# Optimization experiments

Hardware: AMD Instinct MI355X
Metric: run time of the kernel (lower is better)

## Reference

```python
import jax, jax.numpy as jnp
import numpy as np

INPUT_DIM = 1068   # 768 + 300
HIDDEN = 768
KERNEL_SIZES = (3, 5, 7)
NUM_KERNELS = (256, 256, 256)
SPACE = 16
NEG_SLOPE = 0.01   # LeakyReLU default
N_DOCS = 128
MAX_LEN = 200


def _pos_encoding(n_pos, d):
    pos = np.arange(n_pos)[:, None].astype(np.float32)
    i = np.arange(d // 2)[None, :].astype(np.float32)
    angle = pos / np.power(10000.0, 2.0 * i / d)
    pe = np.zeros((n_pos, d), dtype=np.float32)
    pe[:, 0::2] = np.sin(angle)
    pe[:, 1::2] = np.cos(angle)
    return pe

_PE = jnp.asarray(_pos_encoding(MAX_LEN, INPUT_DIM))


def _lstm_cell(x, h, c, W_ih, W_hh, b_ih, b_hh):
    # torch.nn.LSTMCell gate math, gate order i, f, g, o
    g = x @ W_ih.T + b_ih + h @ W_hh.T + b_hh
    i, f, gg, o = jnp.split(g, 4, axis=-1)
    c2 = jax.nn.sigmoid(f) * c + jax.nn.sigmoid(i) * jnp.tanh(gg)
    return jax.nn.sigmoid(o) * jnp.tanh(c2), c2


def _chunked_hidden(xp, W_ih, W_hh, b_ih, b_hh):
    # Replicates getHiddenStates: each chunk of SPACE positions is one batched
    # LSTMCell step; the state at offset j within a chunk carries to offset j of
    # the next chunk (SPACE interleaved recurrences). Padding the tail is safe
    # because padded states are never read back (original slices hx[:len]).
    N, F = xp.shape
    H = W_hh.shape[1]
    n_chunks = -(-N // SPACE)
    pad = n_chunks * SPACE - N
    xk = jnp.pad(xp, ((0, pad), (0, 0))).reshape(n_chunks, SPACE, F)

    def step(carry, xc):
        h, c = carry
        h, c = _lstm_cell(xc, h, c, W_ih, W_hh, b_ih, b_hh)
        return (h, c), (h, c)

    init = (jnp.zeros((SPACE, H), xp.dtype), jnp.zeros((SPACE, H), xp.dtype))
    _, (hs, cs) = jax.lax.scan(step, init, xk)
    return hs.reshape(-1, H)[:N], cs.reshape(-1, H)[:N]


def _maxpool_same(x, k):  # x: [C, L], stride 1, padding k//2 (k odd -> same L)
    p = k // 2
    return jax.lax.reduce_window(x, -jnp.inf, jax.lax.max, (1, k), (1, 1), [(0, 0), (p, p)])


def setup_inputs() -> dict:
    key = jax.random.key(0)
    ks = jax.random.split(key, 16)
    doc_lens = np.asarray(jax.random.randint(ks[0], (N_DOCS,), 50, MAX_LEN))
    L = N_DOCS * MAX_LEN
    inp = {
        "x": jax.random.normal(ks[1], (1, L, INPUT_DIM), jnp.float32),
        "doc_lens": doc_lens,
    }
    for j, (k, oc) in enumerate(zip(KERNEL_SIZES, NUM_KERNELS)):
        inp[f"conv_w{j}"] = jax.random.normal(ks[2 + j], (oc, INPUT_DIM, k), jnp.float32) * 0.02
        inp[f"conv_b{j}"] = jnp.zeros((oc,), jnp.float32)
    F = sum(NUM_KERNELS)
    for name, kk in (("", ks[6]), ("_rev", ks[7])):
        k1, k2 = jax.random.split(kk)
        inp[f"W_ih{name}"] = jax.random.normal(k1, (4 * HIDDEN, F), jnp.float32) * 0.05
        inp[f"W_hh{name}"] = jax.random.normal(k2, (4 * HIDDEN, HIDDEN), jnp.float32) * 0.05
        inp[f"b_ih{name}"] = jnp.zeros((4 * HIDDEN,), jnp.float32)
        inp[f"b_hh{name}"] = jnp.zeros((4 * HIDDEN,), jnp.float32)
    return inp


def reference(x, doc_lens, conv_w0, conv_b0, conv_w1, conv_b1, conv_w2, conv_b2,
              W_ih, W_hh, b_ih, b_hh, W_ih_rev, W_hh_rev, b_ih_rev, b_hh_rev):
    doc_lens = np.asarray(doc_lens)
    N = int(doc_lens.sum())
    pos_idx = np.concatenate([np.arange(int(l)) for l in doc_lens])  # per-doc positions

    x_doc = x[0, :N] + _PE[pos_idx]                 # [N, D]
    xc = x_doc.T[None]                              # [1, D, N]

    convs, pools = [], []
    for w, b, k in ((conv_w0, conv_b0, 3), (conv_w1, conv_b1, 5), (conv_w2, conv_b2, 7)):
        p = (k - 1) // 2  # 'same' padding for odd k
        y = jax.lax.conv_general_dilated(xc, w, (1,), [(p, p)],
                                         dimension_numbers=("NCH", "OIH", "NCH"))[0] + b[:, None]
        y = jnp.where(y >= 0, y, NEG_SLOPE * y)     # LeakyReLU
        convs.append(y)
        pools.append(_maxpool_same(y, k))
    x_feat = jnp.concatenate(convs, axis=0).T       # [N, sumK]
    x_pooled = jnp.concatenate(pools, axis=0).T     # [N, sumK]

    h, c = _chunked_hidden(x_pooled, W_ih, W_hh, b_ih, b_hh)
    # NOTE: the original also runs getHiddenStates on the reversed sequence with
    # lstm_rev (h_rev, c_rev) but never uses the result -> dead code, omitted.

    min_dis = SPACE // 2 + 1
    z = jnp.zeros((min_dis, HIDDEN), h.dtype)
    h_prev = jnp.concatenate([z, h[:N - min_dis]], axis=0)   # h[i-min_dis] or 0
    c_prev = jnp.concatenate([z, c[:N - min_dis]], axis=0)
    h_next = jnp.concatenate([h[min_dis:], z], axis=0)       # h[i+min_dis] or 0
    c_next = jnp.concatenate([c[min_dis:], z], axis=0)

    hi, _ = _lstm_cell(x_feat, h_prev, c_prev, W_ih, W_hh, b_ih, b_hh)
    hi_rev, _ = _lstm_cell(x_feat, h_next, c_next, W_ih_rev, W_hh_rev, b_ih_rev, b_hh_rev)
    return jnp.concatenate([hi, hi_rev], axis=-1)[None]      # [1, N, 2H]
```

## Files before the change

kernel.cpp:

```cpp
#include <hip/hip_runtime.h>
#include <hip/hip_bf16.h>
#include <hip/hip_fp16.h>
#include <math.h>

#define DIN   1068
#define DPAD  1088
#define HID   768
#define G4    3072
#define NWG_SCAN 96
#define SLAB  2048
#define HPAD  776
#define GBM   128
#define GBN   128
#define AROWP 40

typedef _Float16 half8 __attribute__((ext_vector_type(8)));
typedef float    floatx4 __attribute__((ext_vector_type(4)));

__device__ __forceinline__ float sigf(float x){ return 1.0f/(1.0f + expf(-x)); }

__global__ void k_prep(const int* __restrict__ doc_lens, int* __restrict__ pos_idx, int N){
    __shared__ int off[129];
    if (threadIdx.x == 0){
        int a = 0;
        for (int d = 0; d < 128; ++d){ off[d] = a; a += doc_lens[d]; }
        off[128] = a;
    }
    __syncthreads();
    for (int d = threadIdx.x; d < 128; d += blockDim.x){
        int s = off[d], e = off[d+1];
        for (int n = s; n < e && n < N; ++n) pos_idx[n] = n - s;
    }
}

__global__ void k_fill_xdoc(const float* __restrict__ x, const int* __restrict__ pos_idx,
                            float* __restrict__ xd, int N){
    int idx = blockIdx.x*256 + threadIdx.x;
    int total = N * DPAD;
    if (idx >= total) return;
    int n = idx / DPAD;
    int d = idx - n*DPAD;
    float v = 0.f;
    if (d < DIN){
        int pos = pos_idx[n];
        int i2 = d & ~1;
        float ex  = expf(-(float)i2 * (9.210340371976184f / 1068.0f));
        float ang = (float)pos * ex;
        v = x[(size_t)n*DIN + d] + ((d & 1) ? cosf(ang) : sinf(ang));
    }
    xd[(size_t)(n+4)*DPAD + d] = v;
}

__global__ void k_repack_w(const float* __restrict__ w0, const float* __restrict__ w1,
                           const float* __restrict__ w2, float* __restrict__ wrep){
    int idx = blockIdx.x*256 + threadIdx.x;
    const int total = 15*256*DPAD;
    if (idx >= total) return;
    int d    = idx % DPAD;
    int rest = idx / DPAD;
    int oc   = rest % 256;
    int tau  = rest / 256;
    const float* w; int k, t;
    if (tau < 3)      { w = w0; k = 3; t = tau;     }
    else if (tau < 8) { w = w1; k = 5; t = tau - 3; }
    else              { w = w2; k = 7; t = tau - 8; }
    float v = 0.f;
    if (d < DIN) v = w[((size_t)oc*DIN + d)*k + t];
    wrep[(size_t)idx] = v;
}

template<bool SPLIT>
__device__ __forceinline__ void mfma_core(
    const float* __restrict__ A, const float* __restrict__ B, int K,
    int m0, int shift, int rowcap, int tid, floatx4 (&acc)[4][4],
    _Float16* __restrict__ Ahi, _Float16* __restrict__ Alo,
    _Float16* __restrict__ Bhi, _Float16* __restrict__ Blo)
{
    const int st_r = tid >> 1;
    const int st_s = (tid & 1) * 16;
    const int wv = tid >> 6, lane = tid & 63;
    const int wr = wv >> 1, wc = wv & 1;
    const int mloc = lane & 15, kb = lane >> 4;
    for (int k0 = 0; k0 < K; k0 += 32){
        {
            float av[16] = {};
            int r = m0 + st_r + shift;
            if ((unsigned)r < (unsigned)rowcap){
                const float* pa = A + (size_t)r*K + k0 + st_s;
                *(float4*)&av[0]  = *(const float4*)pa;
                *(float4*)&av[4]  = *(const float4*)(pa+4);
                *(float4*)&av[8]  = *(const float4*)(pa+8);
                *(float4*)&av[12] = *(const float4*)(pa+12);
            }
            #pragma unroll
            for (int g = 0; g < 2; ++g){
                half8 hh, hl;
                #pragma unroll
                for (int e = 0; e < 8; ++e){
                    float f = av[g*8+e];
                    _Float16 h = (_Float16)f;
                    hh[e] = h;
                    if (SPLIT) hl[e] = (_Float16)(f - (float)h);
                }
                *(half8*)&Ahi[st_r*AROWP + st_s + g*8] = hh;
                if (SPLIT) *(half8*)&Alo[st_r*AROWP + st_s + g*8] = hl;
            }
        }
        {
            float bv[16];
            const float* pb = B + (size_t)st_r*K + k0 + st_s;
            *(float4*)&bv[0]  = *(const float4*)pb;
            *(float4*)&bv[4]  = *(const float4*)(pb+4);
            *(float4*)&bv[8]  = *(const float4*)(pb+8);
            *(float4*)&bv[12] = *(const float4*)(pb+12);
            #pragma unroll
            for (int g = 0; g < 2; ++g){
                half8 hh, hl;
                #pragma unroll
                for (int e = 0; e < 8; ++e){
                    float f = bv[g*8+e];
                    _Float16 h = (_Float16)f;
                    hh[e] = h;
                    if (SPLIT) hl[e] = (_Float16)(f - (float)h);
                }
                *(half8*)&Bhi[st_r*AROWP + st_s + g*8] = hh;
                if (SPLIT) *(half8*)&Blo[st_r*AROWP + st_s + g*8] = hl;
            }
        }
        __syncthreads();
        half8 afh[4], bfh[4], afl[4], bfl[4];
        #pragma unroll
        for (int i = 0; i < 4; ++i){
            afh[i] = *(const half8*)&Ahi[(wr*64 + i*16 + mloc)*AROWP + kb*8];
            bfh[i] = *(const half8*)&Bhi[(wc*64 + i*16 + mloc)*AROWP + kb*8];
            if (SPLIT){
                afl[i] = *(const half8*)&Alo[(wr*64 + i*16 + mloc)*AROWP + kb*8];
                bfl[i] = *(const half8*)&Blo[(wc*64 + i*16 + mloc)*AROWP + kb*8];
            }
        }
        #pragma unroll
        for (int i = 0; i < 4; ++i)
            #pragma unroll
            for (int j = 0; j < 4; ++j){
                acc[i][j] = __builtin_amdgcn_mfma_f32_16x16x32_f16(afh[i], bfh[j], acc[i][j], 0, 0, 0);
                if (SPLIT){
                    acc[i][j] = __builtin_amdgcn_mfma_f32_16x16x32_f16(afh[i], bfl[j], acc[i][j], 0, 0, 0);
                    acc[i][j] = __builtin_amdgcn_mfma_f32_16x16x32_f16(afl[i], bfh[j], acc[i][j], 0, 0, 0);
                }
            }
        __syncthreads();
    }
}

template<bool CHALF>
__global__ __launch_bounds__(256) void k_gemm_split(
    const float* __restrict__ A0, const float* __restrict__ B0,
    const float* __restrict__ bias0, const float* __restrict__ bias1,
    void* __restrict__ C, int M, int K, int ldc)
{
    __shared__ _Float16 Ahi[GBM*AROWP], Alo[GBM*AROWP];
    __shared__ _Float16 Bhi[GBN*AROWP], Blo[GBN*AROWP];
    floatx4 zz = {0.f, 0.f, 0.f, 0.f};
    floatx4 acc[4][4];
    #pragma unroll
    for (int i = 0; i < 4; ++i)
        #pragma unroll
        for (int j = 0; j < 4; ++j) acc[i][j] = zz;
    const int tid = threadIdx.x;
    const int m0 = blockIdx.x*GBM;
    const int n0 = blockIdx.y*GBN;
    mfma_core<true>(A0, B0 + (size_t)n0*K, K, m0, 0, M, tid, acc, Ahi, Alo, Bhi, Blo);
    const int wv = tid >> 6, lane = tid & 63;
    const int wr = wv >> 1, wc = wv & 1;
    const int mloc = lane & 15, kb = lane >> 4;
    float bv[4];
    #pragma unroll
    for (int j = 0; j < 4; ++j){
        int cn = n0 + wc*64 + j*16 + mloc;
        bv[j] = bias0[cn] + (bias1 ? bias1[cn] : 0.f);
    }
    #pragma unroll
    for (int i = 0; i < 4; ++i){
        #pragma unroll
        for (int r = 0; r < 4; ++r){
            int gm = m0 + wr*64 + i*16 + kb*4 + r;
            if (gm >= M) continue;
            #pragma unroll
            for (int j = 0; j < 4; ++j){
                int cn = n0 + wc*64 + j*16 + mloc;
                float v = acc[i][j][r] + bv[j];
                if (CHALF) ((__half*)C)[(size_t)gm*ldc + cn] = __float2half(v);
                else       ((float*)C)[(size_t)gm*ldc + cn] = v;
            }
        }
    }
}

__global__ __launch_bounds__(256) void k_gemm_plain2(
    const float* __restrict__ A0, const float* __restrict__ B0,
    const float* __restrict__ A1, const float* __restrict__ B1,
    const float* __restrict__ bias0, const float* __restrict__ bias1,
    float* __restrict__ C, int M, int K, int ldc)
{
    __shared__ _Float16 Ahi[GBM*AROWP];
    __shared__ _Float16 Bhi[GBN*AROWP];
    floatx4 zz = {0.f, 0.f, 0.f, 0.f};
    floatx4 acc[4][4];
    #pragma unroll
    for (int i = 0; i < 4; ++i)
        #pragma unroll
        for (int j = 0; j < 4; ++j) acc[i][j] = zz;
    const int tid = threadIdx.x;
    const int m0 = blockIdx.x*GBM;
    const int n0 = blockIdx.y*GBN;
    mfma_core<false>(A0, B0 + (size_t)n0*K, K, m0, 0, M, tid, acc, Ahi, nullptr, Bhi, nullptr);
    mfma_core<false>(A1, B1 + (size_t)n0*K, K, m0, 0, M, tid, acc, Ahi, nullptr, Bhi, nullptr);
    const int wv = tid >> 6, lane = tid & 63;
    const int wr = wv >> 1, wc = wv & 1;
    const int mloc = lane & 15, kb = lane >> 4;
    float bv[4];
    #pragma unroll
    for (int j = 0; j < 4; ++j){
        int cn = n0 + wc*64 + j*16 + mloc;
        bv[j] = bias0[cn] + bias1[cn];
    }
    #pragma unroll
    for (int i = 0; i < 4; ++i){
        #pragma unroll
        for (int r = 0; r < 4; ++r){
            int gm = m0 + wr*64 + i*16 + kb*4 + r;
            if (gm >= M) continue;
            #pragma unroll
            for (int j = 0; j < 4; ++j){
                int cn = n0 + wc*64 + j*16 + mloc;
                C[(size_t)gm*ldc + cn] = acc[i][j][r] + bv[j];
            }
        }
    }
}

__global__ __launch_bounds__(256) void k_conv_gemm(
    const float* __restrict__ xd, const float* __restrict__ wrep,
    const float* __restrict__ cb0, const float* __restrict__ cb1, const float* __restrict__ cb2,
    float* __restrict__ x_feat, int N)
{
    __shared__ _Float16 Ahi[GBM*AROWP], Alo[GBM*AROWP];
    __shared__ _Float16 Bhi[GBN*AROWP], Blo[GBN*AROWP];
    floatx4 zz = {0.f, 0.f, 0.f, 0.f};
    floatx4 acc[4][4];
    #pragma unroll
    for (int i = 0; i < 4; ++i)
        #pragma unroll
        for (int j = 0; j < 4; ++j) acc[i][j] = zz;
    const int tid = threadIdx.x;
    const int m0  = blockIdx.x*GBM;
    const int gid = blockIdx.y;
    const int g = gid >> 1, half = gid & 1;
    const int kg = (g==0)?3:((g==1)?5:7);
    const int p  = kg >> 1;
    const int tb = (g==0)?0:((g==1)?3:8);
    for (int t = 0; t < kg; ++t){
        const float* B = wrep + ((size_t)(tb + t)*256 + half*128)*DPAD;
        mfma_core<true>(xd, B, DPAD, m0, 4 + t - p, N + 8, tid, acc, Ahi, Alo, Bhi, Blo);
    }
    const float* cb = (g==0)?cb0:((g==1)?cb1:cb2);
    const int wv = tid >> 6, lane = tid & 63;
    const int wr = wv >> 1, wc = wv & 1;
    const int mloc = lane & 15, kb = lane >> 4;
    float bv[4];
    #pragma unroll
    for (int j = 0; j < 4; ++j) bv[j] = cb[half*128 + wc*64 + j*16 + mloc];
    const int colbase = g*256 + half*128 + wc*64 + mloc;
    #pragma unroll
    for (int i = 0; i < 4; ++i){
        #pragma unroll
        for (int r = 0; r < 4; ++r){
            int gm = m0 + wr*64 + i*16 + kb*4 + r;
            if (gm >= N) continue;
            float* crow = x_feat + (size_t)gm*HID + colbase;
            #pragma unroll
            for (int j = 0; j < 4; ++j){
                float y = acc[i][j][r] + bv[j];
                crow[j*16] = (y >= 0.f) ? y : 0.01f*y;
            }
        }
    }
}

__global__ void k_pool(const float* __restrict__ xf, float* __restrict__ xp, int N){
    int idx = blockIdx.x*256 + threadIdx.x;
    if (idx >= N*HID) return;
    int n = idx / HID, ch = idx - n*HID;
    int p = (ch < 256) ? 1 : ((ch < 512) ? 2 : 3);
    float m = -INFINITY;
    for (int d = -p; d <= p; ++d){
        int r = n + d;
        if (0 <= r && r < N) m = fmaxf(m, xf[(size_t)r*HID + ch]);
    }
    xp[idx] = m;
}

__global__ __launch_bounds__(256, 1) void k_scan(
    const __half* __restrict__ G1, const float* __restrict__ W_hh,
    float* __restrict__ h_all, __half* __restrict__ c_all,
    __half* __restrict__ h_buf, unsigned int* __restrict__ flags,
    int N, int n_chunks)
{
    __shared__ __align__(16) __half hs16[16*HPAD];
    __shared__ float gbuf[2][32][17];
    const int w    = blockIdx.x;
    const int t    = threadIdx.x;
    const int lane = t & 63;
    const int wv   = t >> 6;
    const int mt   = wv & 1;
    const int kh   = wv >> 1;
    const int mloc = lane & 15;
    const int kb   = lane >> 4;
    const int mg   = mt*16 + mloc;
    const int qq   = mg >> 3;
    const int il   = mg & 7;
    const int grow = qq*HID + w*8 + il;
    half8 areg[12];
    #pragma unroll
    for (int sk = 0; sk < 12; ++sk){
        const float* wp = W_hh + (size_t)grow*HID + kh*384 + sk*32 + kb*8;
        half8 a;
        #pragma unroll
        for (int e = 0; e < 8; ++e) a[e] = (_Float16)wp[e];
        areg[sk] = a;
    }
    float cstate = 0.f;
    const int ci = t >> 4;
    const int cc = t & 15;
    const int st_row = t >> 4;
    const int st_wq  = (t & 15) * 12;
    for (int s = 0; s < n_chunks; ++s){
        float g1v0=0.f, g1v1=0.f, g1v2=0.f, g1v3=0.f;
        int n = s*16 + cc;
        if (t < 128 && n < N){
            const __half* g1r = G1 + (size_t)n*G4 + w*8 + ci;
            g1v0 = __half2float(g1r[0]);
            g1v1 = __half2float(g1r[HID]);
            g1v2 = __half2float(g1r[2*HID]);
            g1v3 = __half2float(g1r[3*HID]);
        }
        {
            const unsigned long long* hsrc =
                (const unsigned long long*)(h_buf + (size_t)(s & 1)*(16*HID))
                + (size_t)st_row*192 + st_wq;
            unsigned long long tmp[12];
            #pragma unroll
            for (int i = 0; i < 12; ++i)
                tmp[i] = __hip_atomic_load(hsrc + i, __ATOMIC_RELAXED,
                                           __HIP_MEMORY_SCOPE_AGENT);
            unsigned long long* hrow =
                (unsigned long long*)(hs16 + (size_t)st_row*HPAD) + st_wq;
            #pragma unroll
            for (int i = 0; i < 12; ++i) hrow[i] = tmp[i];
        }
        __syncthreads();
        {
            floatx4 acc = {0.f, 0.f, 0.f, 0.f};
            const _Float16* hb = (const _Float16*)hs16;
            #pragma unroll
            for (int sk = 0; sk < 12; ++sk){
                int k0 = kh*384 + sk*32 + kb*8;
                half8 b = *(const half8*)(hb + (size_t)mloc*HPAD + k0);
                acc = __builtin_amdgcn_mfma_f32_16x16x32_f16(areg[sk], b, acc, 0, 0, 0);
            }
            #pragma unroll
            for (int r = 0; r < 4; ++r)
                gbuf[kh][mt*16 + kb*4 + r][mloc] = acc[r];
        }
        __syncthreads();
        if (t < 128 && n < N){
            int col = w*8 + ci;
            float gI = gbuf[0][0*8+ci][cc] + gbuf[1][0*8+ci][cc] + g1v0;
            float gF = gbuf[0][1*8+ci][cc] + gbuf[1][1*8+ci][cc] + g1v1;
            float gG = gbuf[0][2*8+ci][cc] + gbuf[1][2*8+ci][cc] + g1v2;
            float gO = gbuf[0][3*8+ci][cc] + gbuf[1][3*8+ci][cc] + g1v3;
            float c2 = sigf(gF)*cstate + sigf(gI)*tanhf(gG);
            float h2 = sigf(gO)*tanhf(c2);
            cstate = c2;
            size_t rowoff = (size_t)(16 + n)*HID + col;
            h_all[rowoff] = h2;
            c_all[rowoff] = __float2half(c2);
            unsigned hb2 = (unsigned)__half_as_ushort(__float2half(h2));
            unsigned other = __shfl_xor(hb2, 16, 64);
            if ((ci & 1) == 0){
                unsigned pk = hb2 | (other << 16);
                unsigned* dst = (unsigned*)h_buf +
                    (((size_t)((s+1)&1)*(16*HID) + (size_t)cc*HID + col) >> 1);
                __hip_atomic_store(dst, pk, __ATOMIC_RELAXED, __HIP_MEMORY_SCOPE_AGENT);
            }
        }
        __syncthreads();
        if (t == 0)
            __hip_atomic_store(&flags[w*16], (unsigned)(s + 1),
                               __ATOMIC_RELAXED, __HIP_MEMORY_SCOPE_AGENT);
        if (t < NWG_SCAN){
            while (__hip_atomic_load(&flags[t*16], __ATOMIC_RELAXED,
                                     __HIP_MEMORY_SCOPE_AGENT) < (unsigned)(s + 1))
                __builtin_amdgcn_s_sleep(1);
        }
        __syncthreads();
    }
}

__global__ void k_cell(const float* __restrict__ g2, const float* __restrict__ g3,
                       const __half* __restrict__ c_all, float* __restrict__ out,
                       int n0, int Mslab, int N){
    int idx = blockIdx.x*256 + threadIdx.x;
    if (idx >= Mslab*HID) return;
    int nl = idx / HID, j = idx - nl*HID;
    int n = n0 + nl;
    const float* r2 = g2 + (size_t)nl*G4;
    float cp = __half2float(c_all[(size_t)(7 + n)*HID + j]);
    float c2 = sigf(r2[HID + j])*cp + sigf(r2[j])*tanhf(r2[2*HID + j]);
    out[(size_t)n*1536 + j] = sigf(r2[3*HID + j])*tanhf(c2);
    const float* r3 = g3 + (size_t)nl*G4;
    float cn = __half2float(c_all[(size_t)(25 + n)*HID + j]);
    float c3 = sigf(r3[HID + j])*cn + sigf(r3[j])*tanhf(r3[2*HID + j]);
    out[(size_t)n*1536 + HID + j] = sigf(r3[3*HID + j])*tanhf(c3);
}

extern "C" void kernel_launch(void* const* d_in, const int* in_sizes, int n_in,
                              void* d_out, int out_size, void* d_ws, size_t ws_size,
                              hipStream_t stream)
{
    const float* x     = (const float*)d_in[0];
    const int*   dl    = (const int*)  d_in[1];
    const float* cw0   = (const float*)d_in[2];
    const float* cb0   = (const float*)d_in[3];
    const float* cw1   = (const float*)d_in[4];
    const float* cb1   = (const float*)d_in[5];
    const float* cw2   = (const float*)d_in[6];
    const float* cb2   = (const float*)d_in[7];
    const float* W_ih  = (const float*)d_in[8];
    const float* W_hh  = (const float*)d_in[9];
    const float* b_ih  = (const float*)d_in[10];
    const float* b_hh  = (const float*)d_in[11];
    const float* W_ihr = (const float*)d_in[12];
    const float* W_hhr = (const float*)d_in[13];
    const float* b_ihr = (const float*)d_in[14];
    const float* b_hhr = (const float*)d_in[15];
    float* out = (float*)d_out;
    (void)in_sizes; (void)n_in;
    const int N = out_size / (2*HID);
    if (N <= 0) return;
    const int n_chunks = (N + 15)/16;
    const int N16 = n_chunks*16;

    auto AL = [](size_t b){ return (b + 255) & ~(size_t)255; };
    const size_t szXd   = AL((size_t)(N+8)*DPAD*4);
    const size_t szW    = AL((size_t)15*256*DPAD*4);
    const size_t szPool = AL((size_t)N*HID*4);
    const size_t szH    = AL((size_t)(N+32)*HID*4);
    const size_t szC    = AL((size_t)(N+32)*HID*2);
    size_t r0 = szXd + szW;
    if (szPool     > r0) r0 = szPool;
    if (szH + szC  > r0) r0 = szH + szC;
    const size_t szF    = AL((size_t)N*HID*4);
    size_t szG1 = AL((size_t)N16*G4*2);
    const size_t szGG   = AL((size_t)SLAB*G4*4);
    if (2*szGG > szG1) szG1 = 2*szGG;
    const size_t szHB   = AL((size_t)2*16*HID*2);
    const size_t szFL   = AL((size_t)NWG_SCAN*16*4);
    const size_t szPI   = AL((size_t)N*4);

    char* wsb = (char*)d_ws;
    size_t off = 0;
    char* R0   = wsb;              off += r0;
    char* pF   = wsb + off;        off += szF;
    char* pG1  = wsb + off;        off += szG1;
    char* pHB  = wsb + off;        off += szHB;
    char* pFL  = wsb + off;        off += szFL;
    char* pPI  = wsb + off;        off += szPI;
    if (off > ws_size) return;

    float*          xd    = (float*)R0;
    float*          wrep  = (float*)(R0 + szXd);
    float*          x_pool= (float*)R0;
    float*          h_all = (float*)R0;
    __half*         c_all = (__half*)(R0 + szH);
    float*          x_feat= (float*)pF;
    __half*         G1    = (__half*)pG1;
    float*          g2    = (float*)pG1;
    float*          g3    = (float*)(pG1 + szGG);
    __half*         h_buf = (__half*)pHB;
    unsigned*       flags = (unsigned*)pFL;
    int*            pos_idx = (int*)pPI;

    hipMemsetAsync(xd, 0, (size_t)4*DPAD*4, stream);
    hipMemsetAsync(xd + (size_t)(N+4)*DPAD, 0, (size_t)4*DPAD*4, stream);
    k_prep<<<1, 128, 0, stream>>>(dl, pos_idx, N);
    k_fill_xdoc<<<(N*DPAD + 255)/256, 256, 0, stream>>>(x, pos_idx, xd, N);
    k_repack_w<<<(15*256*DPAD + 255)/256, 256, 0, stream>>>(cw0, cw1, cw2, wrep);

    const int mt = (N + GBM - 1)/GBM;
    k_conv_gemm<<<dim3(mt, 6), 256, 0, stream>>>(xd, wrep, cb0, cb1, cb2, x_feat, N);
    k_pool<<<(N*HID + 255)/256, 256, 0, stream>>>(x_feat, x_pool, N);

    k_gemm_split<true><<<dim3(mt, G4/GBN), 256, 0, stream>>>(
        x_pool, W_ih, b_ih, b_hh, G1, N, HID, G4);

    hipMemsetAsync(h_all, 0, (size_t)16*HID*4, stream);
    hipMemsetAsync(h_all + (size_t)(16+N)*HID, 0, (size_t)16*HID*4, stream);
    hipMemsetAsync(c_all, 0, (size_t)16*HID*2, stream);
    hipMemsetAsync(c_all + (size_t)(16+N)*HID, 0, (size_t)16*HID*2, stream);
    hipMemsetAsync(h_buf, 0, (size_t)2*16*HID*2, stream);
    hipMemsetAsync(flags, 0, szFL, stream);
    k_scan<<<NWG_SCAN, 256, 0, stream>>>(G1, W_hh, h_all, c_all, h_buf, flags, N, n_chunks);

    for (int n0 = 0; n0 < N; n0 += SLAB){
        int ms  = (N - n0 < SLAB) ? (N - n0) : SLAB;
        int mts = (ms + GBM - 1)/GBM;
        k_gemm_plain2<<<dim3(mts, G4/GBN), 256, 0, stream>>>(
            x_feat + (size_t)n0*HID, W_ih, h_all + (size_t)(7+n0)*HID, W_hh,
            b_ih, b_hh, g2, ms, HID, G4);
        k_gemm_plain2<<<dim3(mts, G4/GBN), 256, 0, stream>>>(
            x_feat + (size_t)n0*HID, W_ihr, h_all + (size_t)(25+n0)*HID, W_hhr,
            b_ihr, b_hhr, g3, ms, HID, G4);
        k_cell<<<(ms*HID + 255)/256, 256, 0, stream>>>(g2, g3, c_all, out, n0, ms, N);
    }
}
```

Baseline: 6.606 ms.

## Replace per-step flag barrier with step-tagged hidden-state words in scan

The recurrent scan kernel no longer synchronises its 96 workgroups with a flag array, a spin loop and two extra block barriers per step. Each packed fp16 hidden pair is now stored together with its step number in one 64-bit atomic word, and readers spin until every word they need carries the expected tag. This removes a global barrier round trip from the serial critical path. In exchange the hidden-state buffer doubles in size and each thread polls 24 words instead of one flag.

Measured after the change: 15.87 ms. +140.2%, slower.

```diff
diff --git a/kernel.cpp b/kernel.cpp
--- a/kernel.cpp
+++ b/kernel.cpp
@@ -303,7 +303,7 @@
 __global__ __launch_bounds__(256, 1) void k_scan(
     const __half* __restrict__ G1, const float* __restrict__ W_hh,
     float* __restrict__ h_all, __half* __restrict__ c_all,
-    __half* __restrict__ h_buf, unsigned int* __restrict__ flags,
+    unsigned long long* __restrict__ h_buf,
     int N, int n_chunks)
 {
     __shared__ __align__(16) __half hs16[16*HPAD];
@@ -333,7 +333,6 @@
     const int ci = t >> 4;
     const int cc = t & 15;
     const int st_row = t >> 4;
-    const int st_wq  = (t & 15) * 12;
     for (int s = 0; s < n_chunks; ++s){
         float g1v0=0.f, g1v1=0.f, g1v2=0.f, g1v3=0.f;
         int n = s*16 + cc;
@@ -345,18 +344,32 @@
             g1v3 = __half2float(g1r[3*HID]);
         }
         {
-            const unsigned long long* hsrc =
-                (const unsigned long long*)(h_buf + (size_t)(s & 1)*(16*HID))
-                + (size_t)st_row*192 + st_wq;
-            unsigned long long tmp[12];
+            const unsigned want = (unsigned)s;
+            const unsigned long long* src =
+                h_buf + (size_t)(s & 1)*6144 + (size_t)t*24;
+            unsigned long long v[24];
+            #pragma unroll
+            for (int i = 0; i < 24; ++i)
+                v[i] = __hip_atomic_load(src + i, __ATOMIC_RELAXED,
+                                         __HIP_MEMORY_SCOPE_AGENT);
+            for (;;){
+                bool ok = true;
+                #pragma unroll
+                for (int i = 0; i < 24; ++i)
+                    ok &= ((unsigned)(v[i] >> 32) == want);
+                if (ok) break;
+                __builtin_amdgcn_s_sleep(1);
+                #pragma unroll
+                for (int i = 0; i < 24; ++i)
+                    if ((unsigned)(v[i] >> 32) != want)
+                        v[i] = __hip_atomic_load(src + i, __ATOMIC_RELAXED,
+                                                 __HIP_MEMORY_SCOPE_AGENT);
+            }
+            unsigned long long* hrow =
+                (unsigned long long*)(hs16 + (size_t)st_row*HPAD) + (t & 15)*12;
             #pragma unroll
             for (int i = 0; i < 12; ++i)
-                tmp[i] = __hip_atomic_load(hsrc + i, __ATOMIC_RELAXED,
-                                           __HIP_MEMORY_SCOPE_AGENT);
-            unsigned long long* hrow =
-                (unsigned long long*)(hs16 + (size_t)st_row*HPAD) + st_wq;
-            #pragma unroll
-            for (int i = 0; i < 12; ++i) hrow[i] = tmp[i];
+                hrow[i] = (v[2*i] & 0xffffffffull) | (v[2*i+1] << 32);
         }
         __syncthreads();
         {
@@ -373,37 +386,35 @@
                 gbuf[kh][mt*16 + kb*4 + r][mloc] = acc[r];
         }
         __syncthreads();
-        if (t < 128 && n < N){
-            int col = w*8 + ci;
-            float gI = gbuf[0][0*8+ci][cc] + gbuf[1][0*8+ci][cc] + g1v0;
-            float gF = gbuf[0][1*8+ci][cc] + gbuf[1][1*8+ci][cc] + g1v1;
-            float gG = gbuf[0][2*8+ci][cc] + gbuf[1][2*8+ci][cc] + g1v2;
-            float gO = gbuf[0][3*8+ci][cc] + gbuf[1][3*8+ci][cc] + g1v3;
-            float c2 = sigf(gF)*cstate + sigf(gI)*tanhf(gG);
-            float h2 = sigf(gO)*tanhf(c2);
-            cstate = c2;
-            size_t rowoff = (size_t)(16 + n)*HID + col;
-            h_all[rowoff] = h2;
-            c_all[rowoff] = __float2half(c2);
+        if (t < 128){
+            float h2 = 0.f;
+            if (n < N){
+                int col = w*8 + ci;
+                float gI = gbuf[0][0*8+ci][cc] + gbuf[1][0*8+ci][cc] + g1v0;
+                float gF = gbuf[0][1*8+ci][cc] + gbuf[1][1*8+ci][cc] + g1v1;
+                float gG = gbuf[0][2*8+ci][cc] + gbuf[1][2*8+ci][cc] + g1v2;
+                float gO = gbuf[0][3*8+ci][cc] + gbuf[1][3*8+ci][cc] + g1v3;
+                float c2 = sigf(gF)*cstate + sigf(gI)*tanhf(gG);
+                h2 = sigf(gO)*tanhf(c2);
+                cstate = c2;
+                size_t rowoff = (size_t)(16 + n)*HID + col;
+                h_all[rowoff] = h2;
+                c_all[rowoff] = __float2half(c2);
+            }
             unsigned hb2 = (unsigned)__half_as_ushort(__float2half(h2));
             unsigned other = __shfl_xor(hb2, 16, 64);
             if ((ci & 1) == 0){
                 unsigned pk = hb2 | (other << 16);
-                unsigned* dst = (unsigned*)h_buf +
-                    (((size_t)((s+1)&1)*(16*HID) + (size_t)cc*HID + col) >> 1);
-                __hip_atomic_store(dst, pk, __ATOMIC_RELAXED, __HIP_MEMORY_SCOPE_AGENT);
-            }
-        }
-        __syncthreads();
-        if (t == 0)
-            __hip_atomic_store(&flags[w*16], (unsigned)(s + 1),
-                               __ATOMIC_RELAXED, __HIP_MEMORY_SCOPE_AGENT);
-        if (t < NWG_SCAN){
-            while (__hip_atomic_load(&flags[t*16], __ATOMIC_RELAXED,
-                                     __HIP_MEMORY_SCOPE_AGENT) < (unsigned)(s + 1))
-                __builtin_amdgcn_s_sleep(1);
-        }
-        __syncthreads();
+                unsigned long long word =
+                    (unsigned long long)pk |
+                    ((unsigned long long)(unsigned)(s + 1) << 32);
+                unsigned long long* dst =
+                    h_buf + (size_t)((s+1) & 1)*6144 +
+                    (size_t)cc*384 + (size_t)w*4 + (ci >> 1);
+                __hip_atomic_store(dst, word, __ATOMIC_RELAXED,
+                                   __HIP_MEMORY_SCOPE_AGENT);
+            }
+        }
     }
 }
 
@@ -464,8 +475,7 @@
     size_t szG1 = AL((size_t)N16*G4*2);
     const size_t szGG   = AL((size_t)SLAB*G4*4);
     if (2*szGG > szG1) szG1 = 2*szGG;
-    const size_t szHB   = AL((size_t)2*16*HID*2);
-    const size_t szFL   = AL((size_t)NWG_SCAN*16*4);
+    const size_t szHB   = AL((size_t)2*6144*8);
     const size_t szPI   = AL((size_t)N*4);
 
     char* wsb = (char*)d_ws;
@@ -474,22 +484,20 @@
     char* pF   = wsb + off;        off += szF;
     char* pG1  = wsb + off;        off += szG1;
     char* pHB  = wsb + off;        off += szHB;
-    char* pFL  = wsb + off;        off += szFL;
     char* pPI  = wsb + off;        off += szPI;
     if (off > ws_size) return;
 
-    float*          xd    = (float*)R0;
-    float*          wrep  = (float*)(R0 + szXd);
-    float*          x_pool= (float*)R0;
-    float*          h_all = (float*)R0;
-    __half*         c_all = (__half*)(R0 + szH);
-    float*          x_feat= (float*)pF;
-    __half*         G1    = (__half*)pG1;
-    float*          g2    = (float*)pG1;
-    float*          g3    = (float*)(pG1 + szGG);
-    __half*         h_buf = (__half*)pHB;
-    unsigned*       flags = (unsigned*)pFL;
-    int*            pos_idx = (int*)pPI;
+    float*              xd    = (float*)R0;
+    float*              wrep  = (float*)(R0 + szXd);
+    float*              x_pool= (float*)R0;
+    float*              h_all = (float*)R0;
+    __half*             c_all = (__half*)(R0 + szH);
+    float*              x_feat= (float*)pF;
+    __half*             G1    = (__half*)pG1;
+    float*              g2    = (float*)pG1;
+    float*              g3    = (float*)(pG1 + szGG);
+    unsigned long long* h_buf = (unsigned long long*)pHB;
+    int*                pos_idx = (int*)pPI;
 
     hipMemsetAsync(xd, 0, (size_t)4*DPAD*4, stream);
     hipMemsetAsync(xd + (size_t)(N+4)*DPAD, 0, (size_t)4*DPAD*4, stream);
@@ -508,9 +516,8 @@
     hipMemsetAsync(h_all + (size_t)(16+N)*HID, 0, (size_t)16*HID*4, stream);
     hipMemsetAsync(c_all, 0, (size_t)16*HID*2, stream);
     hipMemsetAsync(c_all + (size_t)(16+N)*HID, 0, (size_t)16*HID*2, stream);
-    hipMemsetAsync(h_buf, 0, (size_t)2*16*HID*2, stream);
-    hipMemsetAsync(flags, 0, szFL, stream);
-    k_scan<<<NWG_SCAN, 256, 0, stream>>>(G1, W_hh, h_all, c_all, h_buf, flags, N, n_chunks);
+    hipMemsetAsync(h_buf, 0, szHB, stream);
+    k_scan<<<NWG_SCAN, 256, 0, stream>>>(G1, W_hh, h_all, c_all, h_buf, N, n_chunks);
 
     for (int n0 = 0; n0 < N; n0 += SLAB){
         int ms  = (N - n0 < SLAB) ? (N - n0) : SLAB;
```
